# Performance work log

Measured on AMD Instinct MI355X. Metric: run time of the kernel, lower is better.

Reference implementation:

```python
import jax, jax.numpy as jnp
import numpy as np

N = 100_000      # nodes
E = 1_600_000    # edges (avg degree 16)
F_IN = 128       # input feature dim
D = 128          # encoder hidden/output dim
Z_DIM = 64       # learned z parameter width
PE = 4           # laplacian PE dim (pe_projector is Linear(4,4))
T = 4096         # number of target nodes
P_MAX = 131_072  # padded (target, sub_node) pair count
H_PRED = 256     # predictor hidden
D_OUT = 128      # predictor output


def setup_inputs() -> dict:
    key = jax.random.key(0)
    ks = jax.random.split(key, 12)
    rng = np.random.default_rng(0)
    src = rng.integers(0, N, size=E).astype(np.int32)
    dst = rng.integers(0, N, size=E).astype(np.int32)
    targets = rng.permutation(N)[:T].astype(np.int32)
    # flatten the per-target 1-hop subgraph loop into (target_idx, sub_node) pairs
    tpos = np.full(N, -1, np.int64)
    tpos[targets] = np.arange(T)
    sel = tpos[dst] >= 0
    pt = np.concatenate([np.arange(T), tpos[dst[sel]]]).astype(np.int32)  # target index
    ps = np.concatenate([targets, src[sel]]).astype(np.int32)             # sub node id
    p = min(len(pt), P_MAX)
    pair_t = np.zeros(P_MAX, np.int32); pair_t[:p] = pt[:p]
    pair_s = np.zeros(P_MAX, np.int32); pair_s[:p] = ps[:p]
    pair_mask = np.zeros(P_MAX, np.float32); pair_mask[:p] = 1.0

    def w(k, shape, fan):
        return jax.random.normal(k, shape, jnp.float32) * (1.0 / np.sqrt(fan))

    F_PRED = D + Z_DIM + 2 * PE  # 200
    return {
        "x": jax.random.normal(ks[0], (N, F_IN), jnp.float32),
        "masked_x": jax.random.normal(ks[1], (N, F_IN), jnp.float32),
        "pos_enc": jax.random.normal(ks[2], (N, PE), jnp.float32),
        "edge_src": jnp.asarray(src), "edge_dst": jnp.asarray(dst),
        "target_nodes": jnp.asarray(targets),
        "pair_t": jnp.asarray(pair_t), "pair_s": jnp.asarray(pair_s),
        "pair_mask": jnp.asarray(pair_mask),
        "W1t": w(ks[3], (F_IN, D), F_IN), "W2t": w(ks[4], (D, D), D),
        "W1c": w(ks[5], (F_IN, D), F_IN), "W2c": w(ks[6], (D, D), D),
        "Wpe": w(ks[7], (PE, PE), PE),
        "z": w(ks[8], (1, Z_DIM), Z_DIM),
        "Wp1": w(ks[9], (F_PRED, H_PRED), F_PRED), "bp1": jnp.zeros((H_PRED,), jnp.float32),
        "Wp2": w(ks[10], (H_PRED, D_OUT), H_PRED), "bp2": jnp.zeros((D_OUT,), jnp.float32),
    }


def _gcn2(x, src, dst, W1, W2):
    # 2-layer message-passing encoder: linear -> mean-neighbor aggregate -> relu -> linear -> aggregate
    deg = jnp.clip(jax.ops.segment_sum(jnp.ones(src.shape[0], x.dtype), dst, num_segments=N), 1.0, None)

    def agg(h):  # [N, D] -> [N, D]
        return jax.ops.segment_sum(h[src], dst, num_segments=N) / deg[:, None]

    h = jax.nn.relu(agg(x @ W1))
    return agg(h @ W2)


def reference(x, masked_x, pos_enc, edge_src, edge_dst, target_nodes, pair_t, pair_s, pair_mask,
              W1t, W2t, W1c, W2c, Wpe, z, Wp1, bp1, Wp2, bp2):
    # target branch (torch.no_grad + detach)
    target_x = jax.lax.stop_gradient(_gcn2(x, edge_src, edge_dst, W1t, W2t))
    target_embeddings = target_x[target_nodes]  # [T, D]
    # context branch
    ctx = _gcn2(masked_x, edge_src, edge_dst, W1c, W2c)  # [N, D]
    pe = pos_enc @ Wpe.T  # Linear(4,4,bias=False)
    P = pair_t.shape[0]
    # per-pair predictor input: [ctx[s], z, pe_proj[s], pe_proj[t]]
    feat = jnp.concatenate([
        ctx[pair_s],                                  # [P, D]
        jnp.broadcast_to(z, (P, z.shape[1])),         # [P, Z_DIM]
        pe[pair_s],                                   # [P, PE]
        pe[target_nodes[pair_t]],                     # [P, PE]
    ], axis=1)
    pred = jax.nn.relu(feat @ Wp1 + bp1) @ Wp2 + bp2  # [P, D_OUT]
    pred = pred * pair_mask[:, None]                  # zero padded pairs
    return pred, target_embeddings
```

## Files before the change

kernel.cpp:

```cpp
#include <hip/hip_runtime.h>
#include <hip/hip_bf16.h>

#define N_NODES 100000
#define E_EDGES 1600000
#define T_TGT   4096
#define P_PAIRS 131072
#define NCHUNK  98

typedef __bf16 bf16x8 __attribute__((ext_vector_type(8)));
typedef float  f32x4  __attribute__((ext_vector_type(4)));

__device__ __forceinline__ float b2f(unsigned short u) {
  unsigned int x = ((unsigned int)u) << 16;
  return __builtin_bit_cast(float, x);
}
__device__ __forceinline__ unsigned short f2b(float f) {
  unsigned int x = __builtin_bit_cast(unsigned int, f);
  x += 0x7fffu + ((x >> 16) & 1u);
  return (unsigned short)(x >> 16);
}
__device__ __forceinline__ bf16x8 ld8(const unsigned short* p) {
  return *reinterpret_cast<const bf16x8*>(p);
}
__device__ __forceinline__ f32x4 mfma16(bf16x8 a, bf16x8 b, f32x4 c) {
  return __builtin_amdgcn_mfma_f32_16x16x32_bf16(a, b, c, 0, 0, 0);
}
__device__ __forceinline__ float ldf(const void* p, size_t i, bool f32) {
  return f32 ? ((const float*)p)[i] : b2f(((const unsigned short*)p)[i]);
}
__device__ __forceinline__ bf16x8 ld8d(const void* p, size_t elem, bool f32) {
  if (!f32) return ld8((const unsigned short*)p + elem);
  const float* q = (const float*)p + elem;
  union { bf16x8 v; unsigned short s[8]; } u;
#pragma unroll
  for (int j = 0; j < 8; ++j) u.s[j] = f2b(q[j]);
  return u.v;
}

__global__ void k_sniff(const unsigned int* __restrict__ x, int* __restrict__ dflag) {
  unsigned int w = x[(size_t)threadIdx.x * 24001];
  int e = (w >> 7) & 0xff;
  if (e < 90 || e > 140) atomicAdd(dflag, 1);
}

__global__ void k_tmark(const int* __restrict__ tn, char* __restrict__ tmark) {
  int i = blockIdx.x * 256 + threadIdx.x;
  if (i < T_TGT) tmark[tn[i]] = 1;
}

__global__ void k_hist(const int* __restrict__ dst, const int* __restrict__ src,
                       int* __restrict__ cnt, int* __restrict__ rank,
                       const char* __restrict__ tmark, char* __restrict__ smark) {
  for (int e = blockIdx.x * blockDim.x + threadIdx.x; e < E_EDGES;
       e += gridDim.x * blockDim.x) {
    int d = dst[e];
    rank[e] = atomicAdd(&cnt[d], 1);
    if (tmark[d]) smark[src[e]] = 1;
  }
}

__global__ void k_scan_a(const int* __restrict__ cnt, int* __restrict__ part,
                         float* __restrict__ dinv) {
  __shared__ int sd[256];
  int t = threadIdx.x;
  int base = blockIdx.x * 1024 + t * 4;
  int s = 0;
  for (int j = 0; j < 4; ++j) {
    int idx = base + j;
    if (idx < N_NODES) {
      int c = cnt[idx];
      s += c;
      dinv[idx] = 1.0f / (float)max(c, 1);
    }
  }
  sd[t] = s; __syncthreads();
  for (int off = 128; off > 0; off >>= 1) {
    if (t < off) sd[t] += sd[t + off];
    __syncthreads();
  }
  if (t == 0) part[blockIdx.x] = sd[0];
}

__global__ void k_scan_b(int* __restrict__ part, int* __restrict__ offs) {
  int run = 0;
  for (int i = 0; i < NCHUNK; ++i) { int v = part[i]; part[i] = run; run += v; }
  offs[N_NODES] = run;
}

__global__ void k_scan_c(const int* __restrict__ cnt, const int* __restrict__ part,
                         int* __restrict__ offs) {
  __shared__ int sd[256];
  int t = threadIdx.x;
  int base = blockIdx.x * 1024 + t * 4;
  int v[4]; int s = 0;
  for (int j = 0; j < 4; ++j) {
    int idx = base + j;
    v[j] = (idx < N_NODES) ? cnt[idx] : 0;
    s += v[j];
  }
  sd[t] = s; __syncthreads();
  for (int off = 1; off < 256; off <<= 1) {
    int x = (t >= off) ? sd[t - off] : 0;
    __syncthreads();
    sd[t] += x;
    __syncthreads();
  }
  int excl = sd[t] - s + part[blockIdx.x];
  for (int j = 0; j < 4; ++j) {
    int idx = base + j;
    if (idx < N_NODES) { offs[idx] = excl; excl += v[j]; }
  }
}

__global__ void k_fillprep(
    const int* __restrict__ esrc, const int* __restrict__ edst,
    const int* __restrict__ offs, const int* __restrict__ rank,
    int* __restrict__ csr,
    const void* __restrict__ W1t, const void* __restrict__ W2t,
    const void* __restrict__ W1c, const void* __restrict__ W2c,
    unsigned short* __restrict__ w1tT, unsigned short* __restrict__ w2tT,
    unsigned short* __restrict__ w1cT, unsigned short* __restrict__ w2cT,
    const void* __restrict__ Wp1, unsigned short* __restrict__ wp1T,
    const void* __restrict__ Wp2, unsigned short* __restrict__ wp2T,
    const void* __restrict__ z, const void* __restrict__ bp1,
    float* __restrict__ zc, const void* __restrict__ pos,
    const void* __restrict__ wpe, unsigned short* __restrict__ pe,
    const char* __restrict__ tmark, const char* __restrict__ smark,
    int* __restrict__ slist, int* __restrict__ mlist, int* __restrict__ cnts,
    const int* __restrict__ dflag) {
  int bb = blockIdx.x;
  if (bb < 1024) {
    for (int e = bb * 256 + threadIdx.x; e < E_EDGES; e += 1024 * 256)
      csr[offs[edst[e]] + rank[e]] = esrc[e];
    return;
  }
  if (bb >= 1960) {
    int lane = threadIdx.x & 63;
    int base = (bb - 1960) * 256 + threadIdx.x;
#pragma unroll
    for (int k = 0; k < 4; ++k) {
      int n = base + k * 25088;
      bool in = n < N_NODES;
      bool ps = in && smark[n];
      bool pm = in && (tmark[n] | smark[n] | (n == 0));
      unsigned long long ms = __ballot(ps);
      unsigned long long mm = __ballot(pm);
      int bs = 0, bm = 0;
      if (lane == 0) {
        if (ms) bs = atomicAdd(&cnts[0], __popcll(ms));
        if (mm) bm = atomicAdd(&cnts[1], __popcll(mm));
      }
      bs = __shfl(bs, 0); bm = __shfl(bm, 0);
      unsigned long long below = (lane == 63) ? ~0ull >> 1 : (1ull << lane) - 1;
      if (ps) slist[bs + __popcll(ms & below)] = n;
      if (pm) mlist[bm + __popcll(mm & below)] = n;
    }
    return;
  }
  bool f32 = *dflag > 128;
  int b = bb - 1024;
  if (b < 256) {
    int w = b >> 6;
    const void* in = (w == 0) ? W1t : (w == 1) ? W2t : (w == 2) ? W1c : W2c;
    unsigned short* out = (w == 0) ? w1tT : (w == 1) ? w2tT : (w == 2) ? w1cT : w2cT;
    int i = (b & 63) * 256 + threadIdx.x;
    int n = i >> 7, k = i & 127;
    out[i] = f2b(ldf(in, (size_t)k * 128 + n, f32));
  } else if (b < 416) {
    int i = (b - 256) * 256 + threadIdx.x;
    int n = i / 160, k = i % 160;
    float v = 0.f;
    if (k < 128)      v = ldf(Wp1, (size_t)k * 256 + n, f32);
    else if (k < 136) v = ldf(Wp1, (size_t)(k + 64) * 256 + n, f32);
    wp1T[i] = f2b(v);
  } else if (b < 544) {
    int i = (b - 416) * 256 + threadIdx.x;
    int n = i >> 8, k = i & 255;
    int ks = (k & 15) * 16 + (k >> 4);
    wp2T[i] = f2b(ldf(Wp2, (size_t)ks * 128 + n, f32));
  } else if (b == 544) {
    int h = threadIdx.x;
    float acc = ldf(bp1, h, f32);
    for (int k = 0; k < 64; ++k)
      acc += ldf(z, k, f32) * ldf(Wp1, (size_t)(128 + k) * 256 + h, f32);
    zc[h] = acc;
  } else {
    int n = (b - 545) * 256 + threadIdx.x;
    if (n >= N_NODES) return;
    float p[4];
    for (int j = 0; j < 4; ++j) p[j] = ldf(pos, (size_t)n * 4 + j, f32);
    for (int i = 0; i < 4; ++i) {
      float acc = 0.f;
      for (int j = 0; j < 4; ++j) acc += p[j] * ldf(wpe, i * 4 + j, f32);
      pe[(size_t)n * 4 + i] = f2b(acc);
    }
  }
}

__device__ __forceinline__ void acc8(float* a, const uint4 v) {
  a[0] += b2f((unsigned short)(v.x & 0xffffu));
  a[1] += b2f((unsigned short)(v.x >> 16));
  a[2] += b2f((unsigned short)(v.y & 0xffffu));
  a[3] += b2f((unsigned short)(v.y >> 16));
  a[4] += b2f((unsigned short)(v.z & 0xffffu));
  a[5] += b2f((unsigned short)(v.z >> 16));
  a[6] += b2f((unsigned short)(v.w & 0xffffu));
  a[7] += b2f((unsigned short)(v.w >> 16));
}

__device__ __forceinline__ void agg_row(const unsigned short* __restrict__ in,
                                        const int* __restrict__ offs,
                                        const int* __restrict__ csr,
                                        const float* __restrict__ dinv,
                                        unsigned short* __restrict__ out,
                                        int i, int n, int relu, int g, int li) {
  int b = offs[n], e = offs[n + 1];
  float a[8] = {0.f, 0.f, 0.f, 0.f, 0.f, 0.f, 0.f, 0.f};
  int len = e - b;
  int nfull = len >> 4;
  for (int c = 0; c < nfull; ++c) {
    int jb = b + (c << 4) + (g << 2);
    int s0 = csr[jb], s1 = csr[jb + 1], s2 = csr[jb + 2], s3 = csr[jb + 3];
    const uint4 v0 = *reinterpret_cast<const uint4*>(in + (size_t)s0 * 128 + li * 8);
    const uint4 v1 = *reinterpret_cast<const uint4*>(in + (size_t)s1 * 128 + li * 8);
    const uint4 v2 = *reinterpret_cast<const uint4*>(in + (size_t)s2 * 128 + li * 8);
    const uint4 v3 = *reinterpret_cast<const uint4*>(in + (size_t)s3 * 128 + li * 8);
    acc8(a, v0); acc8(a, v1); acc8(a, v2); acc8(a, v3);
  }
  for (int j = b + (nfull << 4) + g; j < e; j += 4) {
    int s = csr[j];
    const uint4 v = *reinterpret_cast<const uint4*>(in + (size_t)s * 128 + li * 8);
    acc8(a, v);
  }
#pragma unroll
  for (int c = 0; c < 8; ++c) {
    a[c] += __shfl_xor(a[c], 16);
    a[c] += __shfl_xor(a[c], 32);
  }
  if (g == 0) {
    float sc = dinv[n];
#pragma unroll
    for (int c = 0; c < 8; ++c) {
      a[c] *= sc;
      if (relu) a[c] = fmaxf(a[c], 0.f);
    }
    uint4 o;
    o.x = (unsigned int)f2b(a[0]) | ((unsigned int)f2b(a[1]) << 16);
    o.y = (unsigned int)f2b(a[2]) | ((unsigned int)f2b(a[3]) << 16);
    o.z = (unsigned int)f2b(a[4]) | ((unsigned int)f2b(a[5]) << 16);
    o.w = (unsigned int)f2b(a[6]) | ((unsigned int)f2b(a[7]) << 16);
    *reinterpret_cast<uint4*>(out + (size_t)i * 128 + li * 8) = o;
  }
}

__global__ void k_agg_b(const unsigned short* __restrict__ t1,
                        const unsigned short* __restrict__ c1,
                        const int* __restrict__ offs, const int* __restrict__ csr,
                        const float* __restrict__ dinv,
                        unsigned short* __restrict__ t2,
                        unsigned short* __restrict__ c2,
                        const int* __restrict__ slist, const int* __restrict__ cnts) {
  const int lane = threadIdx.x & 63;
  const int g = lane >> 4;
  const int li = lane & 15;
  int gw = (blockIdx.x * blockDim.x + threadIdx.x) >> 6;
  int nw = (gridDim.x * blockDim.x) >> 6;
  int total = N_NODES + cnts[0];
  for (int i = gw; i < total; i += nw) {
    if (i < N_NODES) {
      agg_row(c1, offs, csr, dinv, c2, i, i, 1, g, li);
    } else {
      int n = slist[i - N_NODES];
      agg_row(t1, offs, csr, dinv, t2, n, n, 1, g, li);
    }
  }
}

__global__ void k_agg_c(const unsigned short* __restrict__ t2,
                        const unsigned short* __restrict__ c2,
                        const int* __restrict__ offs, const int* __restrict__ csr,
                        const float* __restrict__ dinv,
                        unsigned short* __restrict__ gt,
                        unsigned short* __restrict__ ctxb,
                        const int* __restrict__ tn, const int* __restrict__ mlist,
                        const int* __restrict__ cnts) {
  const int lane = threadIdx.x & 63;
  const int g = lane >> 4;
  const int li = lane & 15;
  int gw = (blockIdx.x * blockDim.x + threadIdx.x) >> 6;
  int nw = (gridDim.x * blockDim.x) >> 6;
  int total = T_TGT + cnts[1];
  for (int i = gw; i < total; i += nw) {
    if (i < T_TGT) {
      agg_row(t2, offs, csr, dinv, gt, i, tn[i], 0, g, li);
    } else {
      int n = mlist[i - T_TGT];
      agg_row(c2, offs, csr, dinv, ctxb, n, n, 0, g, li);
    }
  }
}

template <int NT, int KS>
__device__ __forceinline__ void gemm_in_body(const void* __restrict__ A,
                                             const unsigned short* __restrict__ BT,
                                             unsigned short* __restrict__ C, int m0,
                                             int ldb, bool f32) {
  const int lane = threadIdx.x & 63;
  const int lr = lane & 15;
  const int q = lane >> 4;
  f32x4 acc[NT];
#pragma unroll
  for (int i = 0; i < NT; ++i) acc[i] = f32x4{0.f, 0.f, 0.f, 0.f};
  const size_t abase = (size_t)(m0 + lr) * (KS * 32) + q * 8;
#pragma unroll
  for (int ks = 0; ks < KS; ++ks) {
    bf16x8 a = ld8d(A, abase + ks * 32, f32);
#pragma unroll
    for (int nt = 0; nt < NT; ++nt) {
      bf16x8 b = ld8(BT + (size_t)(nt * 16 + lr) * ldb + ks * 32 + q * 8);
      acc[nt] = mfma16(a, b, acc[nt]);
    }
  }
#pragma unroll
  for (int nt = 0; nt < NT; ++nt)
#pragma unroll
    for (int r = 0; r < 4; ++r)
      C[(size_t)(m0 + q * 4 + r) * (NT * 16) + nt * 16 + lr] = f2b(acc[nt][r]);
}

template <int NT, int KS>
__device__ __forceinline__ void gemm_map_body(const unsigned short* __restrict__ A,
                                              const unsigned short* __restrict__ BT,
                                              unsigned short* __restrict__ C, int m0,
                                              int nM, const int* __restrict__ map,
                                              int ldb) {
  const int lane = threadIdx.x & 63;
  const int lr = lane & 15;
  const int q = lane >> 4;
  int rowA = map[min(m0 + lr, nM - 1)];
  f32x4 acc[NT];
#pragma unroll
  for (int i = 0; i < NT; ++i) acc[i] = f32x4{0.f, 0.f, 0.f, 0.f};
  const unsigned short* arow = A + (size_t)rowA * (KS * 32) + q * 8;
#pragma unroll
  for (int ks = 0; ks < KS; ++ks) {
    bf16x8 a = ld8(arow + ks * 32);
#pragma unroll
    for (int nt = 0; nt < NT; ++nt) {
      bf16x8 b = ld8(BT + (size_t)(nt * 16 + lr) * ldb + ks * 32 + q * 8);
      acc[nt] = mfma16(a, b, acc[nt]);
    }
  }
  int rr = m0 + q * 4;
#pragma unroll
  for (int r = 0; r < 4; ++r) {
    if (rr + r < nM) {
      int rowC = map[rr + r];
#pragma unroll
      for (int nt = 0; nt < NT; ++nt)
        C[(size_t)rowC * (NT * 16) + nt * 16 + lr] = f2b(acc[nt][r]);
    }
  }
}

template <int NT, int KS>
__device__ __forceinline__ void gemm_out_body(const unsigned short* __restrict__ A,
                                              const unsigned short* __restrict__ BT,
                                              void* __restrict__ C, size_t elem_off,
                                              int m0, int ldb, bool f32) {
  const int lane = threadIdx.x & 63;
  const int lr = lane & 15;
  const int q = lane >> 4;
  f32x4 acc[NT];
#pragma unroll
  for (int i = 0; i < NT; ++i) acc[i] = f32x4{0.f, 0.f, 0.f, 0.f};
  const unsigned short* arow = A + (size_t)(m0 + lr) * (KS * 32) + q * 8;
#pragma unroll
  for (int ks = 0; ks < KS; ++ks) {
    bf16x8 a = ld8(arow + ks * 32);
#pragma unroll
    for (int nt = 0; nt < NT; ++nt) {
      bf16x8 b = ld8(BT + (size_t)(nt * 16 + lr) * ldb + ks * 32 + q * 8);
      acc[nt] = mfma16(a, b, acc[nt]);
    }
  }
#pragma unroll
  for (int nt = 0; nt < NT; ++nt)
#pragma unroll
    for (int r = 0; r < 4; ++r) {
      size_t idx = elem_off + (size_t)(m0 + q * 4 + r) * (NT * 16) + nt * 16 + lr;
      if (f32) ((float*)C)[idx] = acc[nt][r];
      else     ((unsigned short*)C)[idx] = f2b(acc[nt][r]);
    }
}

__global__ void __launch_bounds__(256) k_gemm_in2(
    const void* __restrict__ A0, const unsigned short* __restrict__ BT0,
    unsigned short* __restrict__ C0, const void* __restrict__ A1,
    const unsigned short* __restrict__ BT1, unsigned short* __restrict__ C1,
    int M, int nblk, const int* __restrict__ dflag) {
  bool f32 = *dflag > 128;
  const int wid = threadIdx.x >> 6;
  bool sec = blockIdx.x >= nblk;
  int bx = sec ? blockIdx.x - nblk : blockIdx.x;
  int m0 = bx * 64 + wid * 16;
  if (m0 >= M) return;
  if (!sec) gemm_in_body<8, 4>(A0, BT0, C0, m0, 128, f32);
  else      gemm_in_body<8, 4>(A1, BT1, C1, m0, 128, f32);
}

__global__ void __launch_bounds__(256) k_gemm_mix(
    const unsigned short* __restrict__ gt, const unsigned short* __restrict__ w2tT,
    void* __restrict__ outp, size_t elem_off,
    const unsigned short* __restrict__ ctxb, const unsigned short* __restrict__ w2cT,
    const int* __restrict__ mlist, const int* __restrict__ cnts,
    const int* __restrict__ dflag) {
  bool f32 = *dflag > 128;
  const int wid = threadIdx.x >> 6;
  if (blockIdx.x < T_TGT / 64) {
    int m0 = blockIdx.x * 64 + wid * 16;
    gemm_out_body<8, 4>(gt, w2tT, outp, elem_off, m0, 128, f32);
  } else {
    int nM = cnts[1];
    int m0 = (blockIdx.x - T_TGT / 64) * 64 + wid * 16;
    if (m0 >= nM) return;
    gemm_map_body<8, 4>(ctxb, w2cT, const_cast<unsigned short*>(ctxb), m0, nM,
                        mlist, 128);
  }
}

__global__ void __launch_bounds__(256) k_pred(
    const unsigned short* __restrict__ ctx, const unsigned short* __restrict__ pe,
    const int* __restrict__ pair_s, const int* __restrict__ pair_t,
    const int* __restrict__ tn, const unsigned short* __restrict__ w1T,
    const float* __restrict__ zc, const unsigned short* __restrict__ w2T,
    const void* __restrict__ b2, const void* __restrict__ pmask,
    void* __restrict__ out, const int* __restrict__ dflag) {
  bool f32 = *dflag > 128;
  const int tid = threadIdx.x;
  const int base = blockIdx.x * 64;

  if (ldf(pmask, base, f32) == 0.f && ldf(pmask, base + 63, f32) == 0.f) {
    size_t be = (size_t)base * 128;
    if (f32) {
      float4 z4 = {0.f, 0.f, 0.f, 0.f};
      float4* o = reinterpret_cast<float4*>((float*)out + be);
      for (int i = tid; i < 2048; i += 256) o[i] = z4;
    } else {
      uint4 z4 = {0u, 0u, 0u, 0u};
      uint4* o = reinterpret_cast<uint4*>((unsigned short*)out + be);
      for (int i = tid; i < 1024; i += 256) o[i] = z4;
    }
    return;
  }

  __shared__ __align__(16) char smem[50688];
  unsigned short* w1L = (unsigned short*)smem;
  unsigned short* shH = (unsigned short*)smem;
  unsigned short* w2L = (unsigned short*)(smem + 33792);

  const int wid = tid >> 6;
  const int lane = tid & 63;
  const int lr = lane & 15;
  const int q = lane >> 4;
  const int m0 = base + wid * 16;
  const int row = m0 + lr;
  const int s = pair_s[row];
  const int tno = tn[pair_t[row]];
  const unsigned short* ctxrow = ctx + (size_t)s * 128 + q * 8;

  bf16x8 af[5];
#pragma unroll
  for (int ks = 0; ks < 5; ++ks) {
    const int kb = ks * 32 + q * 8;
    if (kb < 128) {
      af[ks] = ld8(ctxrow + ks * 32);
    } else if (kb == 128) {
      union { bf16x8 v; unsigned long long d[2]; } u;
      u.d[0] = *reinterpret_cast<const unsigned long long*>(pe + (size_t)s * 4);
      u.d[1] = *reinterpret_cast<const unsigned long long*>(pe + (size_t)tno * 4);
      af[ks] = u.v;
    } else {
      union { bf16x8 v; unsigned long long d[2]; } u;
      u.d[0] = 0; u.d[1] = 0;
      af[ks] = u.v;
    }
  }

  f32x4 acc[16];
#pragma unroll
  for (int i = 0; i < 16; ++i) acc[i] = f32x4{0.f, 0.f, 0.f, 0.f};
  for (int h = 0; h < 2; ++h) {
#pragma unroll
    for (int it = 0; it < 10; ++it) {
      int idx = it * 256 + tid;
      int r = idx / 20, c8 = idx % 20;
      *reinterpret_cast<uint4*>(w1L + r * 168 + c8 * 8) =
          *reinterpret_cast<const uint4*>(w1T + (size_t)(h * 128 + r) * 160 + c8 * 8);
    }
    __syncthreads();
#pragma unroll
    for (int ks = 0; ks < 5; ++ks)
#pragma unroll
      for (int nt = 0; nt < 8; ++nt) {
        bf16x8 b = ld8(w1L + (nt * 16 + lr) * 168 + ks * 32 + q * 8);
        acc[h * 8 + nt] = mfma16(af[ks], b, acc[h * 8 + nt]);
      }
    __syncthreads();
  }

  float zcv[16];
#pragma unroll
  for (int c = 0; c < 16; ++c) zcv[c] = zc[c * 16 + lr];
#pragma unroll
  for (int r = 0; r < 4; ++r) {
    unsigned int w[8];
#pragma unroll
    for (int p = 0; p < 8; ++p) {
      float v0 = fmaxf(acc[2 * p][r] + zcv[2 * p], 0.f);
      float v1 = fmaxf(acc[2 * p + 1][r] + zcv[2 * p + 1], 0.f);
      w[p] = (unsigned int)f2b(v0) | ((unsigned int)f2b(v1) << 16);
    }
    unsigned short* dstp = shH + (size_t)(wid * 16 + q * 4 + r) * 264 + lr * 16;
    uint4 o0; o0.x = w[0]; o0.y = w[1]; o0.z = w[2]; o0.w = w[3];
    uint4 o1; o1.x = w[4]; o1.y = w[5]; o1.z = w[6]; o1.w = w[7];
    *reinterpret_cast<uint4*>(dstp) = o0;
    *reinterpret_cast<uint4*>(dstp + 8) = o1;
  }
#pragma unroll
  for (int it = 0; it < 4; ++it) {
    int idx = it * 256 + tid;
    int r = idx >> 5, c8 = idx & 31;
    *reinterpret_cast<uint4*>(w2L + r * 264 + c8 * 8) =
        *reinterpret_cast<const uint4*>(w2T + (size_t)r * 256 + c8 * 8);
  }
  __syncthreads();

  bf16x8 af2[8];
  const unsigned short* hrow = shH + (size_t)(wid * 16 + lr) * 264 + q * 8;
#pragma unroll
  for (int ks = 0; ks < 8; ++ks) af2[ks] = ld8(hrow + ks * 32);

  f32x4 acc2[8];
#pragma unroll
  for (int i = 0; i < 8; ++i) acc2[i] = f32x4{0.f, 0.f, 0.f, 0.f};
  for (int ph = 0; ph < 4; ++ph) {
    if (ph) {
      __syncthreads();
#pragma unroll
      for (int it = 0; it < 4; ++it) {
        int idx = it * 256 + tid;
        int r = idx >> 5, c8 = idx & 31;
        *reinterpret_cast<uint4*>(w2L + r * 264 + c8 * 8) =
            *reinterpret_cast<const uint4*>(w2T + (size_t)(ph * 32 + r) * 256 + c8 * 8);
      }
      __syncthreads();
    }
#pragma unroll
    for (int nt2 = 0; nt2 < 2; ++nt2)
#pragma unroll
      for (int ks = 0; ks < 8; ++ks) {
        bf16x8 b = ld8(w2L + (nt2 * 16 + lr) * 264 + ks * 32 + q * 8);
        acc2[ph * 2 + nt2] = mfma16(af2[ks], b, acc2[ph * 2 + nt2]);
      }
  }

#pragma unroll
  for (int nt = 0; nt < 8; ++nt) {
    float bias = ldf(b2, nt * 16 + lr, f32);
#pragma unroll
    for (int r = 0; r < 4; ++r) {
      int rr = m0 + q * 4 + r;
      float mk = ldf(pmask, rr, f32);
      float v = (acc2[nt][r] + bias) * mk;
      size_t idx = (size_t)rr * 128 + nt * 16 + lr;
      if (f32) ((float*)out)[idx] = v;
      else     ((unsigned short*)out)[idx] = f2b(v);
    }
  }
}

extern "C" void kernel_launch(void* const* d_in, const int* in_sizes, int n_in,
                              void* d_out, int out_size, void* d_ws, size_t ws_size,
                              hipStream_t stream) {
  const void* x    = d_in[0];
  const void* mx   = d_in[1];
  const void* pos  = d_in[2];
  const int* esrc  = (const int*)d_in[3];
  const int* edst  = (const int*)d_in[4];
  const int* tn    = (const int*)d_in[5];
  const int* pt    = (const int*)d_in[6];
  const int* ps    = (const int*)d_in[7];
  const void* pmask= d_in[8];
  const void* W1t  = d_in[9];
  const void* W2t  = d_in[10];
  const void* W1c  = d_in[11];
  const void* W2c  = d_in[12];
  const void* Wpe  = d_in[13];
  const void* z    = d_in[14];
  const void* Wp1  = d_in[15];
  const void* bp1  = d_in[16];
  const void* Wp2  = d_in[17];
  const void* bp2  = d_in[18];

  char* w = (char*)d_ws;
  auto carve = [&](size_t bytes) -> void* {
    void* p = (void*)w;
    w += (bytes + 255) & ~(size_t)255;
    return p;
  };
  int*   dflag = (int*)carve(256);
  int*   offs  = (int*)carve((N_NODES + 1) * sizeof(int));
  int*   cur   = (int*)carve(N_NODES * sizeof(int));
  char*  tmark = (char*)carve(N_NODES);
  char*  smark = (char*)carve(N_NODES);
  int*   cnts  = (int*)carve(256);
  size_t zspan = (size_t)((char*)cnts + 256 - (char*)cur);
  int*   part  = (int*)carve(4096);
  int*   csr   = (int*)carve(E_EDGES * sizeof(int));
  float* dinv  = (float*)carve(N_NODES * sizeof(float));
  float* zc    = (float*)carve(256 * sizeof(float));
  int*   slist = (int*)carve(N_NODES * sizeof(int));
  int*   mlist = (int*)carve(N_NODES * sizeof(int));
  unsigned short* t1    = (unsigned short*)carve((size_t)N_NODES * 128 * 2);
  unsigned short* c1    = (unsigned short*)carve((size_t)N_NODES * 128 * 2);
  unsigned short* t2    = (unsigned short*)carve((size_t)N_NODES * 128 * 2);
  unsigned short* c2    = (unsigned short*)carve((size_t)N_NODES * 128 * 2);
  unsigned short* ctxb  = (unsigned short*)carve((size_t)N_NODES * 128 * 2);
  unsigned short* peB   = (unsigned short*)carve((size_t)N_NODES * 4 * 2);
  unsigned short* gt    = (unsigned short*)carve((size_t)T_TGT * 128 * 2);
  unsigned short* w1tT  = (unsigned short*)carve(128 * 128 * 2);
  unsigned short* w2tT  = (unsigned short*)carve(128 * 128 * 2);
  unsigned short* w1cT  = (unsigned short*)carve(128 * 128 * 2);
  unsigned short* w2cT  = (unsigned short*)carve(128 * 128 * 2);
  unsigned short* wp1T  = (unsigned short*)carve(256 * 160 * 2);
  unsigned short* wp2T  = (unsigned short*)carve(128 * 256 * 2);
  int* rank = (int*)t1;

  hipMemsetAsync(dflag, 0, sizeof(int), stream);
  k_sniff<<<1, 256, 0, stream>>>((const unsigned int*)x, dflag);

  hipMemsetAsync(cur, 0, zspan, stream);
  k_tmark<<<16, 256, 0, stream>>>(tn, tmark);
  k_hist<<<1024, 256, 0, stream>>>(edst, esrc, cur, rank, tmark, smark);
  k_scan_a<<<NCHUNK, 256, 0, stream>>>(cur, part, dinv);
  k_scan_b<<<1, 1, 0, stream>>>(part, offs);
  k_scan_c<<<NCHUNK, 256, 0, stream>>>(cur, part, offs);

  k_fillprep<<<2058, 256, 0, stream>>>(esrc, edst, offs, rank, csr,
                                       W1t, W2t, W1c, W2c, w1tT, w2tT, w1cT, w2cT,
                                       Wp1, wp1T, Wp2, wp2T, z, bp1, zc, pos, Wpe,
                                       peB, tmark, smark, slist, mlist, cnts, dflag);

  const int gemmN_grid = (N_NODES + 63) / 64;

  k_gemm_in2<<<2 * gemmN_grid, 256, 0, stream>>>(x, w1tT, t1, mx, w1cT, c1,
                                                 N_NODES, gemmN_grid, dflag);

  k_agg_b<<<8192, 256, 0, stream>>>(t1, c1, offs, csr, dinv, t2, c2, slist, cnts);

  k_agg_c<<<4096, 256, 0, stream>>>(t2, c2, offs, csr, dinv, gt, ctxb, tn, mlist,
                                    cnts);

  k_gemm_mix<<<T_TGT / 64 + gemmN_grid, 256, 0, stream>>>(
      gt, w2tT, d_out, (size_t)P_PAIRS * 128, ctxb, w2cT, mlist, cnts, dflag);

  k_pred<<<P_PAIRS / 64, 256, 0, stream>>>(ctxb, peB, ps, pt, tn, wp1T, zc, wp2T,
                                           bp2, pmask, d_out, dflag);
}
```

Baseline: 573.4 us.

## Regroup preprocessing kernels to cut launches and overlap fill with input GEMM

Merges the sniff and target-mark kernels into one launch, and merges the edge histogram with the weight/PE preparation. It also combines the CSR fill and node-list compaction with the first-layer GEMMs into a single launch so those independent pieces run concurrently. Rank gets its own buffer instead of aliasing t1, because the GEMM now writes t1 while the fill still reads rank. The single memset now spans dflag as well. The aim is fewer launches and serialization gaps, at the cost of extra workspace and heterogeneous blocks sharing one grid.

```diff
diff --git a/kernel.cpp b/kernel.cpp
--- a/kernel.cpp
+++ b/kernel.cpp
@@ -37,85 +37,22 @@
   return u.v;
 }
 
-__global__ void k_sniff(const unsigned int* __restrict__ x, int* __restrict__ dflag) {
-  unsigned int w = x[(size_t)threadIdx.x * 24001];
-  int e = (w >> 7) & 0xff;
-  if (e < 90 || e > 140) atomicAdd(dflag, 1);
-}
-
-__global__ void k_tmark(const int* __restrict__ tn, char* __restrict__ tmark) {
-  int i = blockIdx.x * 256 + threadIdx.x;
-  if (i < T_TGT) tmark[tn[i]] = 1;
-}
-
-__global__ void k_hist(const int* __restrict__ dst, const int* __restrict__ src,
-                       int* __restrict__ cnt, int* __restrict__ rank,
-                       const char* __restrict__ tmark, char* __restrict__ smark) {
-  for (int e = blockIdx.x * blockDim.x + threadIdx.x; e < E_EDGES;
-       e += gridDim.x * blockDim.x) {
-    int d = dst[e];
-    rank[e] = atomicAdd(&cnt[d], 1);
-    if (tmark[d]) smark[src[e]] = 1;
-  }
-}
-
-__global__ void k_scan_a(const int* __restrict__ cnt, int* __restrict__ part,
-                         float* __restrict__ dinv) {
-  __shared__ int sd[256];
-  int t = threadIdx.x;
-  int base = blockIdx.x * 1024 + t * 4;
-  int s = 0;
-  for (int j = 0; j < 4; ++j) {
-    int idx = base + j;
-    if (idx < N_NODES) {
-      int c = cnt[idx];
-      s += c;
-      dinv[idx] = 1.0f / (float)max(c, 1);
-    }
-  }
-  sd[t] = s; __syncthreads();
-  for (int off = 128; off > 0; off >>= 1) {
-    if (t < off) sd[t] += sd[t + off];
-    __syncthreads();
-  }
-  if (t == 0) part[blockIdx.x] = sd[0];
-}
-
-__global__ void k_scan_b(int* __restrict__ part, int* __restrict__ offs) {
-  int run = 0;
-  for (int i = 0; i < NCHUNK; ++i) { int v = part[i]; part[i] = run; run += v; }
-  offs[N_NODES] = run;
-}
-
-__global__ void k_scan_c(const int* __restrict__ cnt, const int* __restrict__ part,
-                         int* __restrict__ offs) {
-  __shared__ int sd[256];
-  int t = threadIdx.x;
-  int base = blockIdx.x * 1024 + t * 4;
-  int v[4]; int s = 0;
-  for (int j = 0; j < 4; ++j) {
-    int idx = base + j;
-    v[j] = (idx < N_NODES) ? cnt[idx] : 0;
-    s += v[j];
-  }
-  sd[t] = s; __syncthreads();
-  for (int off = 1; off < 256; off <<= 1) {
-    int x = (t >= off) ? sd[t - off] : 0;
-    __syncthreads();
-    sd[t] += x;
-    __syncthreads();
-  }
-  int excl = sd[t] - s + part[blockIdx.x];
-  for (int j = 0; j < 4; ++j) {
-    int idx = base + j;
-    if (idx < N_NODES) { offs[idx] = excl; excl += v[j]; }
-  }
-}
-
-__global__ void k_fillprep(
-    const int* __restrict__ esrc, const int* __restrict__ edst,
-    const int* __restrict__ offs, const int* __restrict__ rank,
-    int* __restrict__ csr,
+__global__ void k_pre(const int* __restrict__ tn, char* __restrict__ tmark,
+                      const unsigned int* __restrict__ x, int* __restrict__ dflag) {
+  if (blockIdx.x < 16) {
+    int i = blockIdx.x * 256 + threadIdx.x;
+    if (i < T_TGT) tmark[tn[i]] = 1;
+  } else {
+    unsigned int w = x[(size_t)threadIdx.x * 24001];
+    int e = (w >> 7) & 0xff;
+    if (e < 90 || e > 140) atomicAdd(dflag, 1);
+  }
+}
+
+__global__ void k_histprep(
+    const int* __restrict__ edst, const int* __restrict__ esrc,
+    int* __restrict__ cnt, int* __restrict__ rank,
+    const char* __restrict__ tmark, char* __restrict__ smark,
     const void* __restrict__ W1t, const void* __restrict__ W2t,
     const void* __restrict__ W1c, const void* __restrict__ W2c,
     unsigned short* __restrict__ w1tT, unsigned short* __restrict__ w2tT,
@@ -125,35 +62,13 @@
     const void* __restrict__ z, const void* __restrict__ bp1,
     float* __restrict__ zc, const void* __restrict__ pos,
     const void* __restrict__ wpe, unsigned short* __restrict__ pe,
-    const char* __restrict__ tmark, const char* __restrict__ smark,
-    int* __restrict__ slist, int* __restrict__ mlist, int* __restrict__ cnts,
     const int* __restrict__ dflag) {
   int bb = blockIdx.x;
   if (bb < 1024) {
-    for (int e = bb * 256 + threadIdx.x; e < E_EDGES; e += 1024 * 256)
-      csr[offs[edst[e]] + rank[e]] = esrc[e];
-    return;
-  }
-  if (bb >= 1960) {
-    int lane = threadIdx.x & 63;
-    int base = (bb - 1960) * 256 + threadIdx.x;
-#pragma unroll
-    for (int k = 0; k < 4; ++k) {
-      int n = base + k * 25088;
-      bool in = n < N_NODES;
-      bool ps = in && smark[n];
-      bool pm = in && (tmark[n] | smark[n] | (n == 0));
-      unsigned long long ms = __ballot(ps);
-      unsigned long long mm = __ballot(pm);
-      int bs = 0, bm = 0;
-      if (lane == 0) {
-        if (ms) bs = atomicAdd(&cnts[0], __popcll(ms));
-        if (mm) bm = atomicAdd(&cnts[1], __popcll(mm));
-      }
-      bs = __shfl(bs, 0); bm = __shfl(bm, 0);
-      unsigned long long below = (lane == 63) ? ~0ull >> 1 : (1ull << lane) - 1;
-      if (ps) slist[bs + __popcll(ms & below)] = n;
-      if (pm) mlist[bm + __popcll(mm & below)] = n;
+    for (int e = bb * 256 + threadIdx.x; e < E_EDGES; e += 1024 * 256) {
+      int d = edst[e];
+      rank[e] = atomicAdd(&cnt[d], 1);
+      if (tmark[d]) smark[esrc[e]] = 1;
     }
     return;
   }
@@ -197,6 +112,203 @@
   }
 }
 
+__global__ void k_scan_a(const int* __restrict__ cnt, int* __restrict__ part,
+                         float* __restrict__ dinv) {
+  __shared__ int sd[256];
+  int t = threadIdx.x;
+  int base = blockIdx.x * 1024 + t * 4;
+  int s = 0;
+  for (int j = 0; j < 4; ++j) {
+    int idx = base + j;
+    if (idx < N_NODES) {
+      int c = cnt[idx];
+      s += c;
+      dinv[idx] = 1.0f / (float)max(c, 1);
+    }
+  }
+  sd[t] = s; __syncthreads();
+  for (int off = 128; off > 0; off >>= 1) {
+    if (t < off) sd[t] += sd[t + off];
+    __syncthreads();
+  }
+  if (t == 0) part[blockIdx.x] = sd[0];
+}
+
+__global__ void k_scan_b(int* __restrict__ part, int* __restrict__ offs) {
+  int run = 0;
+  for (int i = 0; i < NCHUNK; ++i) { int v = part[i]; part[i] = run; run += v; }
+  offs[N_NODES] = run;
+}
+
+__global__ void k_scan_c(const int* __restrict__ cnt, const int* __restrict__ part,
+                         int* __restrict__ offs) {
+  __shared__ int sd[256];
+  int t = threadIdx.x;
+  int base = blockIdx.x * 1024 + t * 4;
+  int v[4]; int s = 0;
+  for (int j = 0; j < 4; ++j) {
+    int idx = base + j;
+    v[j] = (idx < N_NODES) ? cnt[idx] : 0;
+    s += v[j];
+  }
+  sd[t] = s; __syncthreads();
+  for (int off = 1; off < 256; off <<= 1) {
+    int x = (t >= off) ? sd[t - off] : 0;
+    __syncthreads();
+    sd[t] += x;
+    __syncthreads();
+  }
+  int excl = sd[t] - s + part[blockIdx.x];
+  for (int j = 0; j < 4; ++j) {
+    int idx = base + j;
+    if (idx < N_NODES) { offs[idx] = excl; excl += v[j]; }
+  }
+}
+
+template <int NT, int KS>
+__device__ __forceinline__ void gemm_in_body(const void* __restrict__ A,
+                                             const unsigned short* __restrict__ BT,
+                                             unsigned short* __restrict__ C, int m0,
+                                             int ldb, bool f32) {
+  const int lane = threadIdx.x & 63;
+  const int lr = lane & 15;
+  const int q = lane >> 4;
+  f32x4 acc[NT];
+#pragma unroll
+  for (int i = 0; i < NT; ++i) acc[i] = f32x4{0.f, 0.f, 0.f, 0.f};
+  const size_t abase = (size_t)(m0 + lr) * (KS * 32) + q * 8;
+#pragma unroll
+  for (int ks = 0; ks < KS; ++ks) {
+    bf16x8 a = ld8d(A, abase + ks * 32, f32);
+#pragma unroll
+    for (int nt = 0; nt < NT; ++nt) {
+      bf16x8 b = ld8(BT + (size_t)(nt * 16 + lr) * ldb + ks * 32 + q * 8);
+      acc[nt] = mfma16(a, b, acc[nt]);
+    }
+  }
+#pragma unroll
+  for (int nt = 0; nt < NT; ++nt)
+#pragma unroll
+    for (int r = 0; r < 4; ++r)
+      C[(size_t)(m0 + q * 4 + r) * (NT * 16) + nt * 16 + lr] = f2b(acc[nt][r]);
+}
+
+template <int NT, int KS>
+__device__ __forceinline__ void gemm_map_body(const unsigned short* __restrict__ A,
+                                              const unsigned short* __restrict__ BT,
+                                              unsigned short* __restrict__ C, int m0,
+                                              int nM, const int* __restrict__ map,
+                                              int ldb) {
+  const int lane = threadIdx.x & 63;
+  const int lr = lane & 15;
+  const int q = lane >> 4;
+  int rowA = map[min(m0 + lr, nM - 1)];
+  f32x4 acc[NT];
+#pragma unroll
+  for (int i = 0; i < NT; ++i) acc[i] = f32x4{0.f, 0.f, 0.f, 0.f};
+  const unsigned short* arow = A + (size_t)rowA * (KS * 32) + q * 8;
+#pragma unroll
+  for (int ks = 0; ks < KS; ++ks) {
+    bf16x8 a = ld8(arow + ks * 32);
+#pragma unroll
+    for (int nt = 0; nt < NT; ++nt) {
+      bf16x8 b = ld8(BT + (size_t)(nt * 16 + lr) * ldb + ks * 32 + q * 8);
+      acc[nt] = mfma16(a, b, acc[nt]);
+    }
+  }
+  int rr = m0 + q * 4;
+#pragma unroll
+  for (int r = 0; r < 4; ++r) {
+    if (rr + r < nM) {
+      int rowC = map[rr + r];
+#pragma unroll
+      for (int nt = 0; nt < NT; ++nt)
+        C[(size_t)rowC * (NT * 16) + nt * 16 + lr] = f2b(acc[nt][r]);
+    }
+  }
+}
+
+template <int NT, int KS>
+__device__ __forceinline__ void gemm_out_body(const unsigned short* __restrict__ A,
+                                              const unsigned short* __restrict__ BT,
+                                              void* __restrict__ C, size_t elem_off,
+                                              int m0, int ldb, bool f32) {
+  const int lane = threadIdx.x & 63;
+  const int lr = lane & 15;
+  const int q = lane >> 4;
+  f32x4 acc[NT];
+#pragma unroll
+  for (int i = 0; i < NT; ++i) acc[i] = f32x4{0.f, 0.f, 0.f, 0.f};
+  const unsigned short* arow = A + (size_t)(m0 + lr) * (KS * 32) + q * 8;
+#pragma unroll
+  for (int ks = 0; ks < KS; ++ks) {
+    bf16x8 a = ld8(arow + ks * 32);
+#pragma unroll
+    for (int nt = 0; nt < NT; ++nt) {
+      bf16x8 b = ld8(BT + (size_t)(nt * 16 + lr) * ldb + ks * 32 + q * 8);
+      acc[nt] = mfma16(a, b, acc[nt]);
+    }
+  }
+#pragma unroll
+  for (int nt = 0; nt < NT; ++nt)
+#pragma unroll
+    for (int r = 0; r < 4; ++r) {
+      size_t idx = elem_off + (size_t)(m0 + q * 4 + r) * (NT * 16) + nt * 16 + lr;
+      if (f32) ((float*)C)[idx] = acc[nt][r];
+      else     ((unsigned short*)C)[idx] = f2b(acc[nt][r]);
+    }
+}
+
+__global__ void __launch_bounds__(256) k_fillgemm(
+    const int* __restrict__ esrc, const int* __restrict__ edst,
+    const int* __restrict__ offs, const int* __restrict__ rank,
+    int* __restrict__ csr,
+    const char* __restrict__ tmark, const char* __restrict__ smark,
+    int* __restrict__ slist, int* __restrict__ mlist, int* __restrict__ cnts,
+    const void* __restrict__ x, const unsigned short* __restrict__ w1tT,
+    unsigned short* __restrict__ t1,
+    const void* __restrict__ mx, const unsigned short* __restrict__ w1cT,
+    unsigned short* __restrict__ c1, int nblk, const int* __restrict__ dflag) {
+  int bb = blockIdx.x;
+  if (bb < 1024) {
+    for (int e = bb * 256 + threadIdx.x; e < E_EDGES; e += 1024 * 256)
+      csr[offs[edst[e]] + rank[e]] = esrc[e];
+    return;
+  }
+  if (bb < 1122) {
+    int lane = threadIdx.x & 63;
+    int base = (bb - 1024) * 256 + threadIdx.x;
+#pragma unroll
+    for (int k = 0; k < 4; ++k) {
+      int n = base + k * 25088;
+      bool in = n < N_NODES;
+      bool ps = in && smark[n];
+      bool pm = in && (tmark[n] | smark[n] | (n == 0));
+      unsigned long long ms = __ballot(ps);
+      unsigned long long mm = __ballot(pm);
+      int bs = 0, bm = 0;
+      if (lane == 0) {
+        if (ms) bs = atomicAdd(&cnts[0], __popcll(ms));
+        if (mm) bm = atomicAdd(&cnts[1], __popcll(mm));
+      }
+      bs = __shfl(bs, 0); bm = __shfl(bm, 0);
+      unsigned long long below = (lane == 63) ? ~0ull >> 1 : (1ull << lane) - 1;
+      if (ps) slist[bs + __popcll(ms & below)] = n;
+      if (pm) mlist[bm + __popcll(mm & below)] = n;
+    }
+    return;
+  }
+  bool f32 = *dflag > 128;
+  const int wid = threadIdx.x >> 6;
+  int b = bb - 1122;
+  bool sec = b >= nblk;
+  int bx = sec ? b - nblk : b;
+  int m0 = bx * 64 + wid * 16;
+  if (m0 >= N_NODES) return;
+  if (!sec) gemm_in_body<8, 4>(x, w1tT, t1, m0, 128, f32);
+  else      gemm_in_body<8, 4>(mx, w1cT, c1, m0, 128, f32);
+}
+
 __device__ __forceinline__ void acc8(float* a, const uint4 v) {
   a[0] += b2f((unsigned short)(v.x & 0xffffu));
   a[1] += b2f((unsigned short)(v.x >> 16));
@@ -298,115 +410,6 @@
       agg_row(c2, offs, csr, dinv, ctxb, n, n, 0, g, li);
     }
   }
-}
-
-template <int NT, int KS>
-__device__ __forceinline__ void gemm_in_body(const void* __restrict__ A,
-                                             const unsigned short* __restrict__ BT,
-                                             unsigned short* __restrict__ C, int m0,
-                                             int ldb, bool f32) {
-  const int lane = threadIdx.x & 63;
-  const int lr = lane & 15;
-  const int q = lane >> 4;
-  f32x4 acc[NT];
-#pragma unroll
-  for (int i = 0; i < NT; ++i) acc[i] = f32x4{0.f, 0.f, 0.f, 0.f};
-  const size_t abase = (size_t)(m0 + lr) * (KS * 32) + q * 8;
-#pragma unroll
-  for (int ks = 0; ks < KS; ++ks) {
-    bf16x8 a = ld8d(A, abase + ks * 32, f32);
-#pragma unroll
-    for (int nt = 0; nt < NT; ++nt) {
-      bf16x8 b = ld8(BT + (size_t)(nt * 16 + lr) * ldb + ks * 32 + q * 8);
-      acc[nt] = mfma16(a, b, acc[nt]);
-    }
-  }
-#pragma unroll
-  for (int nt = 0; nt < NT; ++nt)
-#pragma unroll
-    for (int r = 0; r < 4; ++r)
-      C[(size_t)(m0 + q * 4 + r) * (NT * 16) + nt * 16 + lr] = f2b(acc[nt][r]);
-}
-
-template <int NT, int KS>
-__device__ __forceinline__ void gemm_map_body(const unsigned short* __restrict__ A,
-                                              const unsigned short* __restrict__ BT,
-                                              unsigned short* __restrict__ C, int m0,
-                                              int nM, const int* __restrict__ map,
-                                              int ldb) {
-  const int lane = threadIdx.x & 63;
-  const int lr = lane & 15;
-  const int q = lane >> 4;
-  int rowA = map[min(m0 + lr, nM - 1)];
-  f32x4 acc[NT];
-#pragma unroll
-  for (int i = 0; i < NT; ++i) acc[i] = f32x4{0.f, 0.f, 0.f, 0.f};
-  const unsigned short* arow = A + (size_t)rowA * (KS * 32) + q * 8;
-#pragma unroll
-  for (int ks = 0; ks < KS; ++ks) {
-    bf16x8 a = ld8(arow + ks * 32);
-#pragma unroll
-    for (int nt = 0; nt < NT; ++nt) {
-      bf16x8 b = ld8(BT + (size_t)(nt * 16 + lr) * ldb + ks * 32 + q * 8);
-      acc[nt] = mfma16(a, b, acc[nt]);
-    }
-  }
-  int rr = m0 + q * 4;
-#pragma unroll
-  for (int r = 0; r < 4; ++r) {
-    if (rr + r < nM) {
-      int rowC = map[rr + r];
-#pragma unroll
-      for (int nt = 0; nt < NT; ++nt)
-        C[(size_t)rowC * (NT * 16) + nt * 16 + lr] = f2b(acc[nt][r]);
-    }
-  }
-}
-
-template <int NT, int KS>
-__device__ __forceinline__ void gemm_out_body(const unsigned short* __restrict__ A,
-                                              const unsigned short* __restrict__ BT,
-                                              void* __restrict__ C, size_t elem_off,
-                                              int m0, int ldb, bool f32) {
-  const int lane = threadIdx.x & 63;
-  const int lr = lane & 15;
-  const int q = lane >> 4;
-  f32x4 acc[NT];
-#pragma unroll
-  for (int i = 0; i < NT; ++i) acc[i] = f32x4{0.f, 0.f, 0.f, 0.f};
-  const unsigned short* arow = A + (size_t)(m0 + lr) * (KS * 32) + q * 8;
-#pragma unroll
-  for (int ks = 0; ks < KS; ++ks) {
-    bf16x8 a = ld8(arow + ks * 32);
-#pragma unroll
-    for (int nt = 0; nt < NT; ++nt) {
-      bf16x8 b = ld8(BT + (size_t)(nt * 16 + lr) * ldb + ks * 32 + q * 8);
-      acc[nt] = mfma16(a, b, acc[nt]);
-    }
-  }
-#pragma unroll
-  for (int nt = 0; nt < NT; ++nt)
-#pragma unroll
-    for (int r = 0; r < 4; ++r) {
-      size_t idx = elem_off + (size_t)(m0 + q * 4 + r) * (NT * 16) + nt * 16 + lr;
-      if (f32) ((float*)C)[idx] = acc[nt][r];
-      else     ((unsigned short*)C)[idx] = f2b(acc[nt][r]);
-    }
-}
-
-__global__ void __launch_bounds__(256) k_gemm_in2(
-    const void* __restrict__ A0, const unsigned short* __restrict__ BT0,
-    unsigned short* __restrict__ C0, const void* __restrict__ A1,
-    const unsigned short* __restrict__ BT1, unsigned short* __restrict__ C1,
-    int M, int nblk, const int* __restrict__ dflag) {
-  bool f32 = *dflag > 128;
-  const int wid = threadIdx.x >> 6;
-  bool sec = blockIdx.x >= nblk;
-  int bx = sec ? blockIdx.x - nblk : blockIdx.x;
-  int m0 = bx * 64 + wid * 16;
-  if (m0 >= M) return;
-  if (!sec) gemm_in_body<8, 4>(A0, BT0, C0, m0, 128, f32);
-  else      gemm_in_body<8, 4>(A1, BT1, C1, m0, 128, f32);
 }
 
 __global__ void __launch_bounds__(256) k_gemm_mix(
@@ -610,14 +613,15 @@
     return p;
   };
   int*   dflag = (int*)carve(256);
-  int*   offs  = (int*)carve((N_NODES + 1) * sizeof(int));
   int*   cur   = (int*)carve(N_NODES * sizeof(int));
   char*  tmark = (char*)carve(N_NODES);
   char*  smark = (char*)carve(N_NODES);
   int*   cnts  = (int*)carve(256);
-  size_t zspan = (size_t)((char*)cnts + 256 - (char*)cur);
+  size_t zspan = (size_t)((char*)cnts + 256 - (char*)dflag);
+  int*   offs  = (int*)carve((N_NODES + 1) * sizeof(int));
   int*   part  = (int*)carve(4096);
   int*   csr   = (int*)carve(E_EDGES * sizeof(int));
+  int*   rank  = (int*)carve(E_EDGES * sizeof(int));
   float* dinv  = (float*)carve(N_NODES * sizeof(float));
   float* zc    = (float*)carve(256 * sizeof(float));
   int*   slist = (int*)carve(N_NODES * sizeof(int));
@@ -635,27 +639,24 @@
   unsigned short* w2cT  = (unsigned short*)carve(128 * 128 * 2);
   unsigned short* wp1T  = (unsigned short*)carve(256 * 160 * 2);
   unsigned short* wp2T  = (unsigned short*)carve(128 * 256 * 2);
-  int* rank = (int*)t1;
-
-  hipMemsetAsync(dflag, 0, sizeof(int), stream);
-  k_sniff<<<1, 256, 0, stream>>>((const unsigned int*)x, dflag);
-
-  hipMemsetAsync(cur, 0, zspan, stream);
-  k_tmark<<<16, 256, 0, stream>>>(tn, tmark);
-  k_hist<<<1024, 256, 0, stream>>>(edst, esrc, cur, rank, tmark, smark);
+
+  hipMemsetAsync(dflag, 0, zspan, stream);
+  k_pre<<<17, 256, 0, stream>>>(tn, tmark, (const unsigned int*)x, dflag);
+
+  k_histprep<<<1960, 256, 0, stream>>>(edst, esrc, cur, rank, tmark, smark,
+                                       W1t, W2t, W1c, W2c, w1tT, w2tT, w1cT, w2cT,
+                                       Wp1, wp1T, Wp2, wp2T, z, bp1, zc, pos, Wpe,
+                                       peB, dflag);
+
   k_scan_a<<<NCHUNK, 256, 0, stream>>>(cur, part, dinv);
   k_scan_b<<<1, 1, 0, stream>>>(part, offs);
   k_scan_c<<<NCHUNK, 256, 0, stream>>>(cur, part, offs);
 
-  k_fillprep<<<2058, 256, 0, stream>>>(esrc, edst, offs, rank, csr,
-                                       W1t, W2t, W1c, W2c, w1tT, w2tT, w1cT, w2cT,
-                                       Wp1, wp1T, Wp2, wp2T, z, bp1, zc, pos, Wpe,
-                                       peB, tmark, smark, slist, mlist, cnts, dflag);
-
   const int gemmN_grid = (N_NODES + 63) / 64;
 
-  k_gemm_in2<<<2 * gemmN_grid, 256, 0, stream>>>(x, w1tT, t1, mx, w1cT, c1,
-                                                 N_NODES, gemmN_grid, dflag);
+  k_fillgemm<<<1122 + 2 * gemmN_grid, 256, 0, stream>>>(
+      esrc, edst, offs, rank, csr, tmark, smark, slist, mlist, cnts,
+      x, w1tT, t1, mx, w1cT, c1, gemmN_grid, dflag);
 
   k_agg_b<<<8192, 256, 0, stream>>>(t1, c1, offs, csr, dinv, t2, c2, slist, cnts);
 
```

New measurement: 549.8 us. 1.04x faster.
